# Optimization experiments

Measured on AMD Instinct MI355X. Metric: run time of the kernel, lower is better.

Reference implementation:

```python
import jax, jax.numpy as jnp
import numpy as np

N, D, E, EDGE_DIM, HID4 = 8192, 128, 262144, 50, 32


def setup_inputs() -> dict:
    key = jax.random.key(0)
    k = jax.random.split(key, 8)
    return {
        "mag": jax.random.uniform(k[0], (N, D), dtype=jnp.float32),
        "phase": jax.random.normal(k[1], (N, D), dtype=jnp.float32),
        "edge_index": jax.random.randint(k[2], (2, E), 0, N, dtype=jnp.int64),
        "rbf": jax.random.uniform(k[3], (E, EDGE_DIM), dtype=jnp.float32),
        "W1": jax.random.normal(k[4], (EDGE_DIM, HID4), dtype=jnp.float32) * 0.1,
        "b1": jnp.zeros((HID4,), dtype=jnp.float32),
        "W2": jax.random.normal(k[5], (HID4, 1), dtype=jnp.float32) * 0.1,
        "b2": jnp.zeros((1,), dtype=jnp.float32),
    }


def reference(mag, phase, edge_index, rbf, W1, b1, W2, b2):
    # score_ij = sum_d |z_i||z_j| cos(theta_i - theta_j) / sqrt(D)
    # cos(a-b) identity: = (mag*cos(phase)) @ (mag*cos(phase))^T + (mag*sin)@(mag*sin)^T
    scale = jnp.sqrt(jnp.asarray(mag.shape[-1], mag.dtype))
    a = mag * jnp.cos(phase)  # [N, D]
    b = mag * jnp.sin(phase)  # [N, D]
    scores = (a @ a.T + b @ b.T) / scale  # [N, N]
    # edge bias: Linear -> SiLU -> Linear -> scalar, scattered onto (i, j)
    h = jax.nn.silu(rbf @ W1 + b1)       # [E, HID4]
    bias = (h @ W2 + b2)[:, 0]           # [E]
    scores = scores.at[edge_index[0], edge_index[1]].add(bias)
    attn = jax.nn.softmax(scores, axis=1)  # softmax over keys j
    new_mag = attn @ mag
    new_phase = attn @ phase
    return new_mag, new_phase
```

## Files before the change

### kernel.cpp

```cpp
#include <hip/hip_runtime.h>
#include <hip/hip_bf16.h>

#define NN 8192
#define DD 128
#define DQK 256
#define EE 262144
#define EDGE_DIM 50
#define HID 32
#define CAP 96
#define SCALE 0.08838834764831845f
#define SCALE_LOG2E 0.12752455522410585f

using f32x4 = __attribute__((ext_vector_type(4))) float;
using f32x2 = __attribute__((ext_vector_type(2))) float;
using bf16x8 = __attribute__((ext_vector_type(8))) short;
using s16x4 = __attribute__((ext_vector_type(4))) short;

static __device__ __forceinline__ short f2b(float f) {
  __hip_bfloat16 h = __float2bfloat16(f);
  return __builtin_bit_cast(short, h);
}
static __device__ __forceinline__ float b2f(short s) {
  unsigned u = ((unsigned)(unsigned short)s) << 16;
  return __builtin_bit_cast(float, u);
}
static __device__ __forceinline__ void gll(const short* g, short* l) {
  __builtin_amdgcn_global_load_lds(
      (const __attribute__((address_space(1))) void*)g,
      (__attribute__((address_space(3))) void*)l, 16, 0, 0);
}

__global__ __launch_bounds__(256) void k1_mega(
    const float* __restrict__ mag, const float* __restrict__ phase,
    short* __restrict__ qkb, short* __restrict__ vtb, short* __restrict__ vb16,
    const float* __restrict__ rbf, const float* __restrict__ W1,
    const float* __restrict__ b1, const float* __restrict__ W2,
    const float* __restrict__ b2, const int* __restrict__ eidx,
    float* __restrict__ bias, int* __restrict__ cnt, int* __restrict__ slot) {
  __shared__ float tile[64][65];
  int b = blockIdx.x;
  int tid = threadIdx.x;
  if (b < 4096) {
    int t = b * 256 + tid;
    int n = t >> 7, d = t & 127;
    float m = mag[t], p = phase[t];
    float sn, cs;
    __sincosf(p, &sn, &cs);
    qkb[(size_t)n * DQK + d] = f2b(m * cs);
    qkb[(size_t)n * DQK + 128 + d] = f2b(m * sn);
    vb16[(size_t)n * DQK + d] = f2b(m);
    vb16[(size_t)n * DQK + 128 + d] = f2b(p);
    return;
  }
  if (b < 4608) {
    int r = b - 4096;
    int bn = r & 127, bd = (r >> 7) & 1, sel = r >> 8;
    const float* src = sel ? phase : mag;
#pragma unroll
    for (int rep = 0; rep < 16; ++rep) {
      int idx = rep * 256 + tid;
      int rr = idx >> 6, c = idx & 63;
      tile[rr][c] = src[(size_t)(bn * 64 + rr) * DD + bd * 64 + c];
    }
    __syncthreads();
#pragma unroll
    for (int rep = 0; rep < 16; ++rep) {
      int idx = rep * 256 + tid;
      int rr = idx >> 6, c = idx & 63;
      vtb[(size_t)(sel * 128 + bd * 64 + rr) * NN + bn * 64 + c] = f2b(tile[c][rr]);
    }
    return;
  }
  int e = (b - 4608) * 256 + tid;
  const float* rrow = rbf + (size_t)e * EDGE_DIM;
  f32x4 r4[12];
#pragma unroll
  for (int k = 0; k < 12; ++k) r4[k] = *reinterpret_cast<const f32x4*>(rrow + 4 * k);
  f32x2 rt2 = *reinterpret_cast<const f32x2*>(rrow + 48);
  float h[HID];
#pragma unroll
  for (int jj = 0; jj < HID; ++jj) h[jj] = b1[jj];
#pragma unroll
  for (int k = 0; k < 48; ++k) {
    float r = r4[k >> 2][k & 3];
#pragma unroll
    for (int jj = 0; jj < HID; ++jj) h[jj] += r * W1[k * HID + jj];
  }
#pragma unroll
  for (int jj = 0; jj < HID; ++jj)
    h[jj] += rt2.x * W1[48 * HID + jj] + rt2.y * W1[49 * HID + jj];
  float outv = b2[0];
#pragma unroll
  for (int jj = 0; jj < HID; ++jj) {
    float x = h[jj];
    outv += W2[jj] * (x / (1.0f + __expf(-x)));
  }
  bias[e] = outv;
  int i = eidx[e];
  int p = atomicAdd(&cnt[i], 1);
  if (p < CAP) slot[i * CAP + p] = e;
}

constexpr int TBM = 64;
constexpr int TBN = 128;

template <int NSPLIT>
__global__ __launch_bounds__(512, 4) void k5_flash(
    const short* __restrict__ qk,
    const short* __restrict__ vt,
    float* __restrict__ nump,
    float* __restrict__ denp) {
  constexpr int QCOLS = NN / NSPLIT;
  constexpr int NCHUNK = QCOLS / TBN;
  constexpr int GPQ = 8 / NSPLIT;
  __shared__ alignas(16) short Qs[TBM * 256];
  __shared__ alignas(16) short KV[2 * TBN * 64];
  __shared__ alignas(16) short Ps[TBM * 128];
  int b = blockIdx.x;
  int q = (b & 7) / GPQ;
  int rb = (b >> 3) * GPQ + (b & (GPQ - 1));
  int tid = threadIdx.x;
  int w = tid >> 6, lane = tid & 63;
  int wr = w >> 2, wc = w & 3;
  int l15 = lane & 15, quad = lane >> 4;
  int rsw = l15 & 7;
  int wbase = w * 64;
  int r0 = rb * TBM;
  int cbase = q * QCOLS;

#pragma unroll
  for (int p = 0; p < 4; ++p) {
    int idx = p * 512 + tid;
    int row = idx >> 5, gs = idx & 31;
    gll(qk + (size_t)(r0 + row) * DQK + ((gs ^ (row & 7)) * 8),
        &Qs[(p * 512 + wbase) * 8]);
  }

  f32x4 o[2][4] = {};
  float den[2] = {0.f, 0.f};
  __syncthreads();

  for (int ch = 0; ch < NCHUNK; ++ch) {
    int c0 = cbase + ch * TBN;
#pragma unroll
    for (int p = 0; p < 2; ++p) {
      int idx = p * 512 + tid;
      int col = idx >> 3, gs = idx & 7;
      gll(qk + (size_t)(c0 + col) * DQK + ((gs ^ (col & 7)) * 8),
          &KV[(p * 512 + wbase) * 8]);
    }
    __syncthreads();
    f32x4 s[2][2] = {};
#pragma unroll
    for (int bk = 0; bk < 4; ++bk) {
      int buf = bk & 1;
      if (bk < 3) {
        int nb = buf ^ 1;
#pragma unroll
        for (int p = 0; p < 2; ++p) {
          int idx = p * 512 + tid;
          int col = idx >> 3, gs = idx & 7;
          gll(qk + (size_t)(c0 + col) * DQK + (bk + 1) * 64 + ((gs ^ (col & 7)) * 8),
              &KV[nb * 8192 + (p * 512 + wbase) * 8]);
        }
      }
#pragma unroll
      for (int ks = 0; ks < 2; ++ks) {
        int g = ks * 4 + quad;
        bf16x8 a[2], bb[2];
#pragma unroll
        for (int rt = 0; rt < 2; ++rt)
          a[rt] = *(const bf16x8*)&Qs[(wr * 32 + rt * 16 + l15) * 256 +
                                      ((bk * 8 + g) ^ rsw) * 8];
#pragma unroll
        for (int ct = 0; ct < 2; ++ct)
          bb[ct] = *(const bf16x8*)&KV[buf * 8192 + (wc * 32 + ct * 16 + l15) * 64 +
                                       (g ^ rsw) * 8];
#pragma unroll
        for (int rt = 0; rt < 2; ++rt)
#pragma unroll
          for (int ct = 0; ct < 2; ++ct)
            s[ct][rt] = __builtin_amdgcn_mfma_f32_16x16x32_bf16(bb[ct], a[rt],
                                                                s[ct][rt], 0, 0, 0);
      }
      __syncthreads();
    }
#pragma unroll
    for (int p = 0; p < 4; ++p) {
      int idx = p * 512 + tid;
      int feat = idx >> 3, gs = idx & 7;
      gll(vt + (size_t)feat * NN + c0 + ((gs ^ (feat & 7)) * 8),
          &KV[(p * 512 + wbase) * 8]);
    }
#pragma unroll
    for (int rt = 0; rt < 2; ++rt) {
      int row = wr * 32 + rt * 16 + l15;
#pragma unroll
      for (int ct = 0; ct < 2; ++ct) {
        s16x4 pk;
#pragma unroll
        for (int r = 0; r < 4; ++r) {
          float pv = exp2f(s[ct][rt][r] * SCALE_LOG2E);
          den[rt] += pv;
          pk[r] = f2b(pv);
        }
        int cg = wc * 4 + ct * 2 + (quad >> 1);
        *reinterpret_cast<s16x4*>(
            &Ps[row * 128 + ((cg ^ (row & 7)) * 8 + (quad & 1) * 4)]) = pk;
      }
    }
    __syncthreads();
#pragma unroll
    for (int jb = 0; jb < 2; ++jb) {
      if (jb == 1) {
        __syncthreads();
#pragma unroll
        for (int p = 0; p < 4; ++p) {
          int idx = p * 512 + tid;
          int feat = idx >> 3, gs = idx & 7;
          gll(vt + (size_t)feat * NN + c0 + 64 + ((gs ^ (feat & 7)) * 8),
              &KV[(p * 512 + wbase) * 8]);
        }
        __syncthreads();
      }
#pragma unroll
      for (int ks = 0; ks < 2; ++ks) {
        int g = ks * 4 + quad;
        bf16x8 pa[2], vb[4];
#pragma unroll
        for (int rt = 0; rt < 2; ++rt) {
          int row = wr * 32 + rt * 16 + l15;
          pa[rt] = *(const bf16x8*)&Ps[row * 128 +
                                       (((jb * 8 + g) ^ (row & 7)) * 8)];
        }
#pragma unroll
        for (int ft = 0; ft < 4; ++ft)
          vb[ft] = *(const bf16x8*)&KV[(wc * 64 + ft * 16 + l15) * 64 + (g ^ rsw) * 8];
#pragma unroll
        for (int rt = 0; rt < 2; ++rt)
#pragma unroll
          for (int ft = 0; ft < 4; ++ft)
            o[rt][ft] = __builtin_amdgcn_mfma_f32_16x16x32_bf16(pa[rt], vb[ft],
                                                                o[rt][ft], 0, 0, 0);
      }
    }
    __syncthreads();
  }
  float* npB = nump + (size_t)q * NN * DQK;
#pragma unroll
  for (int rt = 0; rt < 2; ++rt)
#pragma unroll
    for (int ft = 0; ft < 4; ++ft) {
      int row = r0 + wr * 32 + rt * 16 + quad * 4;
      int feat = wc * 64 + ft * 16 + l15;
#pragma unroll
      for (int r = 0; r < 4; ++r)
        npB[(size_t)(row + r) * DQK + feat] = o[rt][ft][r];
    }
  float* dl = reinterpret_cast<float*>(KV);
#pragma unroll
  for (int rt = 0; rt < 2; ++rt) {
    float d = den[rt];
    d += __shfl_xor(d, 16);
    d += __shfl_xor(d, 32);
    if (lane < 16) dl[wc * TBM + wr * 32 + rt * 16 + lane] = d;
  }
  __syncthreads();
  if (tid < TBM) {
    float d = dl[0 * TBM + tid] + dl[1 * TBM + tid] + dl[2 * TBM + tid] +
              dl[3 * TBM + tid];
    denp[q * NN + r0 + tid] = d;
  }
}

__global__ __launch_bounds__(64) void k6_combine(
    const int* __restrict__ eidx, const float* __restrict__ bias,
    const int* __restrict__ cntArr, const int* __restrict__ slot,
    const short* __restrict__ qk, const short* __restrict__ vb16,
    const float* __restrict__ nump, const float* __restrict__ denp,
    float* __restrict__ out, int nsplit) {
  __shared__ short qs[DQK];
  __shared__ int js[CAP];
  __shared__ float bs[CAP];
  __shared__ int keepf[CAP];
  int i = blockIdx.x;
  int lane = threadIdx.x;
  int cnt = cntArr[i];
  if (cnt > CAP) cnt = CAP;
  *reinterpret_cast<s16x4*>(&qs[lane * 4]) =
      *reinterpret_cast<const s16x4*>(qk + (size_t)i * DQK + lane * 4);
  for (int p = lane; p < cnt; p += 64) {
    int e = slot[i * CAP + p];
    js[p] = eidx[EE + e];
    bs[p] = bias[e];
  }
  __syncthreads();
  {
    int myp[2];
    float mybsum[2];
    int mykeep[2];
    int nm = 0;
    for (int p = lane; p < cnt; p += 64) {
      int j = js[p];
      float bsum = bs[p];
      int keep = 1;
      for (int qq = 0; qq < cnt; ++qq) {
        if (qq == p || js[qq] != j) continue;
        if (qq < p) { keep = 0; break; }
        bsum += bs[qq];
      }
      myp[nm] = p; mybsum[nm] = bsum; mykeep[nm] = keep; ++nm;
    }
    __syncthreads();
    for (int k = 0; k < nm; ++k) { bs[myp[k]] = mybsum[k]; keepf[myp[k]] = mykeep[k]; }
    __syncthreads();
  }
  int sub = lane & 15;
  int grp = lane >> 4;
  const bf16x8* qa = reinterpret_cast<const bf16x8*>(qs + sub * 16);
  bf16x8 q0 = qa[0], q1 = qa[1];
  f32x4 acc[4] = {};
  float denc = 0.f;
  for (int p = grp; p < cnt; p += 4) {
    if (!keepf[p]) continue;
    int j = js[p];
    const bf16x8* kb =
        reinterpret_cast<const bf16x8*>(qk + (size_t)j * DQK + sub * 16);
    const bf16x8* vb =
        reinterpret_cast<const bf16x8*>(vb16 + (size_t)j * DQK + sub * 16);
    bf16x8 k0 = kb[0], k1 = kb[1];
    bf16x8 v0 = vb[0], v1 = vb[1];
    float sp = 0.f;
#pragma unroll
    for (int u = 0; u < 8; ++u) sp += b2f(q0[u]) * b2f(k0[u]);
#pragma unroll
    for (int u = 0; u < 8; ++u) sp += b2f(q1[u]) * b2f(k1[u]);
    sp += __shfl_xor(sp, 1);
    sp += __shfl_xor(sp, 2);
    sp += __shfl_xor(sp, 4);
    sp += __shfl_xor(sp, 8);
    float delta = __expf(sp * SCALE) * expm1f(bs[p]);
    denc += delta;
#pragma unroll
    for (int u = 0; u < 4; ++u) {
      acc[0][u] += delta * b2f(v0[u]);
      acc[1][u] += delta * b2f(v0[4 + u]);
      acc[2][u] += delta * b2f(v1[u]);
      acc[3][u] += delta * b2f(v1[4 + u]);
    }
  }
#pragma unroll
  for (int t = 0; t < 4; ++t) {
#pragma unroll
    for (int u = 0; u < 4; ++u) {
      acc[t][u] += __shfl_xor(acc[t][u], 16);
      acc[t][u] += __shfl_xor(acc[t][u], 32);
    }
  }
  denc += __shfl_xor(denc, 16);
  denc += __shfl_xor(denc, 32);
  int t3 = lane & 3;
  f32x4 sel = (t3 == 0) ? acc[0] : (t3 == 1) ? acc[1] : (t3 == 2) ? acc[2] : acc[3];
  int srcLane = lane >> 2;
  f32x4 a;
#pragma unroll
  for (int u = 0; u < 4; ++u) a[u] = __shfl(sel[u], srcLane);
  float den = denc;
  for (int qq = 0; qq < nsplit; ++qq) {
    const float* np = nump + ((size_t)qq * NN + i) * DQK + lane * 4;
    a += *reinterpret_cast<const f32x4*>(np);
    den += denp[qq * NN + i];
  }
  float inv = 1.0f / den;
  a *= inv;
  float* dst = (lane < 32) ? (out + (size_t)i * DD + lane * 4)
                           : (out + (size_t)NN * DD + (size_t)i * DD + lane * 4 - 128);
  *reinterpret_cast<f32x4*>(dst) = a;
}

constexpr size_t OFF_QK = 0;
constexpr size_t OFF_VT = (size_t)NN * DQK * 2;
constexpr size_t OFF_VB16 = OFF_VT + (size_t)DQK * NN * 2;
constexpr size_t OFF_BIAS = OFF_VB16 + (size_t)NN * DQK * 2;
constexpr size_t OFF_CNT = OFF_BIAS + (size_t)EE * 4;
constexpr size_t OFF_SLOT = OFF_CNT + (size_t)NN * 4;
constexpr size_t OFF_NUMP = (OFF_SLOT + (size_t)NN * CAP * 4 + 255) & ~(size_t)255;
constexpr size_t WS_NEED4 = OFF_NUMP + 4ull * NN * DQK * 4 + 4ull * NN * 4;
constexpr size_t WS_NEED2 = OFF_NUMP + 2ull * NN * DQK * 4 + 2ull * NN * 4;

extern "C" void kernel_launch(void* const* d_in, const int* in_sizes, int n_in,
                              void* d_out, int out_size, void* d_ws, size_t ws_size,
                              hipStream_t stream) {
  const float* mag = (const float*)d_in[0];
  const float* phase = (const float*)d_in[1];
  const int* eidx = (const int*)d_in[2];
  const float* rbf = (const float*)d_in[3];
  const float* W1 = (const float*)d_in[4];
  const float* b1 = (const float*)d_in[5];
  const float* W2 = (const float*)d_in[6];
  const float* b2 = (const float*)d_in[7];
  float* out = (float*)d_out;
  char* ws = (char*)d_ws;
  if (ws_size < WS_NEED2) return;
  int nsplit = (ws_size >= WS_NEED4) ? 4 : 2;

  short* qkb = (short*)(ws + OFF_QK);
  short* vtb = (short*)(ws + OFF_VT);
  short* vb16 = (short*)(ws + OFF_VB16);
  float* bias = (float*)(ws + OFF_BIAS);
  int* cnt = (int*)(ws + OFF_CNT);
  int* slot = (int*)(ws + OFF_SLOT);
  float* nump = (float*)(ws + OFF_NUMP);
  float* denp = (float*)(ws + OFF_NUMP + (size_t)nsplit * NN * DQK * 4);

  hipMemsetAsync(cnt, 0, (size_t)NN * 4, stream);
  k1_mega<<<5632, 256, 0, stream>>>(mag, phase, qkb, vtb, vb16, rbf, W1, b1, W2,
                                    b2, eidx, bias, cnt, slot);
  if (nsplit == 4)
    k5_flash<4><<<(NN / TBM) * 4, 512, 0, stream>>>(qkb, vtb, nump, denp);
  else
    k5_flash<2><<<(NN / TBM) * 2, 512, 0, stream>>>(qkb, vtb, nump, denp);
  k6_combine<<<NN, 64, 0, stream>>>(eidx, bias, cnt, slot, qkb, vb16, nump, denp,
                                    out, nsplit);
}
```

Before: 261.9 us.

## Apply edge bias inside flash kernel via per-row merged edge lists

Moves the sparse edge-bias correction out of the combine kernel and into the flash-attention kernel. A new merge kernel deduplicates each row's edges and stores (j, exp(bias)) pairs. The flash kernel then rescales the matching P entries in shared memory before the PV MFMA and corrects the denominator, so the combine step becomes a simple normalize with no K/V gathers or dot products. The cost is an extra launch, a per-chunk scan of each row's edge list plus an additional barrier in the hot loop, and P values rounded to bf16 before the bias multiply.

```diff
diff --git a/kernel.cpp b/kernel.cpp
--- a/kernel.cpp
+++ b/kernel.cpp
@@ -101,6 +101,39 @@
   if (p < CAP) slot[i * CAP + p] = e;
 }
 
+__global__ __launch_bounds__(64) void k2_merge(
+    const int* __restrict__ eidx, const float* __restrict__ bias,
+    const int* __restrict__ cntArr, const int* __restrict__ slot,
+    int2* __restrict__ edgeJB, int* __restrict__ mcnt) {
+  __shared__ int js[CAP];
+  __shared__ float bs[CAP];
+  int i = blockIdx.x;
+  int lane = threadIdx.x;
+  int cnt = cntArr[i];
+  if (cnt > CAP) cnt = CAP;
+  for (int p = lane; p < cnt; p += 64) {
+    int e = slot[i * CAP + p];
+    js[p] = eidx[EE + e];
+    bs[p] = bias[e];
+  }
+  __syncthreads();
+  for (int p = lane; p < cnt; p += 64) {
+    int j = js[p];
+    float bsum = bs[p];
+    int keep = 1;
+    for (int qq = 0; qq < cnt; ++qq) {
+      if (qq == p || js[qq] != j) continue;
+      if (qq < p) { keep = 0; break; }
+      bsum += bs[qq];
+    }
+    int2 v;
+    v.x = j;
+    v.y = __float_as_int(keep ? __expf(bsum) : 1.0f);
+    edgeJB[(size_t)i * CAP + p] = v;
+  }
+  if (lane == 0) mcnt[i] = cnt;
+}
+
 constexpr int TBM = 64;
 constexpr int TBN = 128;
 
@@ -108,6 +141,8 @@
 __global__ __launch_bounds__(512, 4) void k5_flash(
     const short* __restrict__ qk,
     const short* __restrict__ vt,
+    const int2* __restrict__ ejb,
+    const int* __restrict__ mcnt,
     float* __restrict__ nump,
     float* __restrict__ denp) {
   constexpr int QCOLS = NN / NSPLIT;
@@ -127,6 +162,10 @@
   int wbase = w * 64;
   int r0 = rb * TBM;
   int cbase = q * QCOLS;
+  int row8 = tid >> 3, sl0 = tid & 7;
+  int mc = mcnt[r0 + row8];
+  const int2* erow = ejb + (size_t)(r0 + row8) * CAP;
+  float denAcc = 0.f;
 
 #pragma unroll
   for (int p = 0; p < 4; ++p) {
@@ -210,6 +249,20 @@
       }
     }
     __syncthreads();
+    for (int t = sl0; t < mc; t += 8) {
+      int2 jb2 = erow[t];
+      unsigned dj = (unsigned)(jb2.x - c0);
+      if (dj < (unsigned)TBN) {
+        float eb = __int_as_float(jb2.y);
+        if (eb != 1.0f) {
+          short* ps = &Ps[row8 * 128 + (((dj >> 3) ^ (row8 & 7)) * 8 + (int)(dj & 7))];
+          float oldp = b2f(*ps);
+          *ps = f2b(oldp * eb);
+          denAcc += oldp * (eb - 1.0f);
+        }
+      }
+    }
+    __syncthreads();
 #pragma unroll
     for (int jb = 0; jb < 2; ++jb) {
       if (jb == 1) {
@@ -258,6 +311,7 @@
         npB[(size_t)(row + r) * DQK + feat] = o[rt][ft][r];
     }
   float* dl = reinterpret_cast<float*>(KV);
+  float* corr = reinterpret_cast<float*>(KV) + 4 * TBM;
 #pragma unroll
   for (int rt = 0; rt < 2; ++rt) {
     float d = den[rt];
@@ -265,110 +319,27 @@
     d += __shfl_xor(d, 32);
     if (lane < 16) dl[wc * TBM + wr * 32 + rt * 16 + lane] = d;
   }
+  denAcc += __shfl_xor(denAcc, 1);
+  denAcc += __shfl_xor(denAcc, 2);
+  denAcc += __shfl_xor(denAcc, 4);
+  if (sl0 == 0) corr[row8] = denAcc;
   __syncthreads();
   if (tid < TBM) {
     float d = dl[0 * TBM + tid] + dl[1 * TBM + tid] + dl[2 * TBM + tid] +
-              dl[3 * TBM + tid];
+              dl[3 * TBM + tid] + corr[tid];
     denp[q * NN + r0 + tid] = d;
   }
 }
 
-__global__ __launch_bounds__(64) void k6_combine(
-    const int* __restrict__ eidx, const float* __restrict__ bias,
-    const int* __restrict__ cntArr, const int* __restrict__ slot,
-    const short* __restrict__ qk, const short* __restrict__ vb16,
+__global__ __launch_bounds__(64) void k6_norm(
     const float* __restrict__ nump, const float* __restrict__ denp,
     float* __restrict__ out, int nsplit) {
-  __shared__ short qs[DQK];
-  __shared__ int js[CAP];
-  __shared__ float bs[CAP];
-  __shared__ int keepf[CAP];
   int i = blockIdx.x;
   int lane = threadIdx.x;
-  int cnt = cntArr[i];
-  if (cnt > CAP) cnt = CAP;
-  *reinterpret_cast<s16x4*>(&qs[lane * 4]) =
-      *reinterpret_cast<const s16x4*>(qk + (size_t)i * DQK + lane * 4);
-  for (int p = lane; p < cnt; p += 64) {
-    int e = slot[i * CAP + p];
-    js[p] = eidx[EE + e];
-    bs[p] = bias[e];
-  }
-  __syncthreads();
-  {
-    int myp[2];
-    float mybsum[2];
-    int mykeep[2];
-    int nm = 0;
-    for (int p = lane; p < cnt; p += 64) {
-      int j = js[p];
-      float bsum = bs[p];
-      int keep = 1;
-      for (int qq = 0; qq < cnt; ++qq) {
-        if (qq == p || js[qq] != j) continue;
-        if (qq < p) { keep = 0; break; }
-        bsum += bs[qq];
-      }
-      myp[nm] = p; mybsum[nm] = bsum; mykeep[nm] = keep; ++nm;
-    }
-    __syncthreads();
-    for (int k = 0; k < nm; ++k) { bs[myp[k]] = mybsum[k]; keepf[myp[k]] = mykeep[k]; }
-    __syncthreads();
-  }
-  int sub = lane & 15;
-  int grp = lane >> 4;
-  const bf16x8* qa = reinterpret_cast<const bf16x8*>(qs + sub * 16);
-  bf16x8 q0 = qa[0], q1 = qa[1];
-  f32x4 acc[4] = {};
-  float denc = 0.f;
-  for (int p = grp; p < cnt; p += 4) {
-    if (!keepf[p]) continue;
-    int j = js[p];
-    const bf16x8* kb =
-        reinterpret_cast<const bf16x8*>(qk + (size_t)j * DQK + sub * 16);
-    const bf16x8* vb =
-        reinterpret_cast<const bf16x8*>(vb16 + (size_t)j * DQK + sub * 16);
-    bf16x8 k0 = kb[0], k1 = kb[1];
-    bf16x8 v0 = vb[0], v1 = vb[1];
-    float sp = 0.f;
-#pragma unroll
-    for (int u = 0; u < 8; ++u) sp += b2f(q0[u]) * b2f(k0[u]);
-#pragma unroll
-    for (int u = 0; u < 8; ++u) sp += b2f(q1[u]) * b2f(k1[u]);
-    sp += __shfl_xor(sp, 1);
-    sp += __shfl_xor(sp, 2);
-    sp += __shfl_xor(sp, 4);
-    sp += __shfl_xor(sp, 8);
-    float delta = __expf(sp * SCALE) * expm1f(bs[p]);
-    denc += delta;
-#pragma unroll
-    for (int u = 0; u < 4; ++u) {
-      acc[0][u] += delta * b2f(v0[u]);
-      acc[1][u] += delta * b2f(v0[4 + u]);
-      acc[2][u] += delta * b2f(v1[u]);
-      acc[3][u] += delta * b2f(v1[4 + u]);
-    }
-  }
-#pragma unroll
-  for (int t = 0; t < 4; ++t) {
-#pragma unroll
-    for (int u = 0; u < 4; ++u) {
-      acc[t][u] += __shfl_xor(acc[t][u], 16);
-      acc[t][u] += __shfl_xor(acc[t][u], 32);
-    }
-  }
-  denc += __shfl_xor(denc, 16);
-  denc += __shfl_xor(denc, 32);
-  int t3 = lane & 3;
-  f32x4 sel = (t3 == 0) ? acc[0] : (t3 == 1) ? acc[1] : (t3 == 2) ? acc[2] : acc[3];
-  int srcLane = lane >> 2;
-  f32x4 a;
-#pragma unroll
-  for (int u = 0; u < 4; ++u) a[u] = __shfl(sel[u], srcLane);
-  float den = denc;
+  f32x4 a = {0.f, 0.f, 0.f, 0.f};
+  float den = 0.f;
   for (int qq = 0; qq < nsplit; ++qq) {
-    const float* np = nump + ((size_t)qq * NN + i) * DQK + lane * 4;
-    a += *reinterpret_cast<const f32x4*>(np);
+    a += *reinterpret_cast<const f32x4*>(nump + ((size_t)qq * NN + i) * DQK + lane * 4);
     den += denp[qq * NN + i];
   }
   float inv = 1.0f / den;
@@ -384,7 +355,9 @@
 constexpr size_t OFF_BIAS = OFF_VB16 + (size_t)NN * DQK * 2;
 constexpr size_t OFF_CNT = OFF_BIAS + (size_t)EE * 4;
 constexpr size_t OFF_SLOT = OFF_CNT + (size_t)NN * 4;
-constexpr size_t OFF_NUMP = (OFF_SLOT + (size_t)NN * CAP * 4 + 255) & ~(size_t)255;
+constexpr size_t OFF_EJB = (OFF_SLOT + (size_t)NN * CAP * 4 + 255) & ~(size_t)255;
+constexpr size_t OFF_MCNT = OFF_EJB + (size_t)NN * CAP * 8;
+constexpr size_t OFF_NUMP = (OFF_MCNT + (size_t)NN * 4 + 255) & ~(size_t)255;
 constexpr size_t WS_NEED4 = OFF_NUMP + 4ull * NN * DQK * 4 + 4ull * NN * 4;
 constexpr size_t WS_NEED2 = OFF_NUMP + 2ull * NN * DQK * 4 + 2ull * NN * 4;
 
@@ -410,16 +383,18 @@
   float* bias = (float*)(ws + OFF_BIAS);
   int* cnt = (int*)(ws + OFF_CNT);
   int* slot = (int*)(ws + OFF_SLOT);
+  int2* edgeJB = (int2*)(ws + OFF_EJB);
+  int* mcnt = (int*)(ws + OFF_MCNT);
   float* nump = (float*)(ws + OFF_NUMP);
   float* denp = (float*)(ws + OFF_NUMP + (size_t)nsplit * NN * DQK * 4);
 
   hipMemsetAsync(cnt, 0, (size_t)NN * 4, stream);
   k1_mega<<<5632, 256, 0, stream>>>(mag, phase, qkb, vtb, vb16, rbf, W1, b1, W2,
                                     b2, eidx, bias, cnt, slot);
+  k2_merge<<<NN, 64, 0, stream>>>(eidx, bias, cnt, slot, edgeJB, mcnt);
   if (nsplit == 4)
-    k5_flash<4><<<(NN / TBM) * 4, 512, 0, stream>>>(qkb, vtb, nump, denp);
+    k5_flash<4><<<(NN / TBM) * 4, 512, 0, stream>>>(qkb, vtb, edgeJB, mcnt, nump, denp);
   else
-    k5_flash<2><<<(NN / TBM) * 2, 512, 0, stream>>>(qkb, vtb, nump, denp);
-  k6_combine<<<NN, 64, 0, stream>>>(eidx, bias, cnt, slot, qkb, vb16, nump, denp,
-                                    out, nsplit);
-}
+    k5_flash<2><<<(NN / TBM) * 2, 512, 0, stream>>>(qkb, vtb, edgeJB, mcnt, nump, denp);
+  k6_norm<<<NN, 64, 0, stream>>>(nump, denp, out, nsplit);
+}
```

Result: slower. 273.9 us (+4.6%).
